# Optimization experiments

Measured on AMD Instinct MI355X. Metric: run time of the kernel, lower is better.

Reference implementation:

```python
import jax, jax.numpy as jnp
import numpy as np

VOCAB, D, H = 32000, 256, 1024
B, S = 8, 4096
PAD = 0


def setup_inputs() -> dict:
    key = jax.random.key(0)
    ks = jax.random.split(key, 9)
    x = jax.random.randint(ks[0], (B, S), 0, VOCAB)
    emb = jax.random.normal(ks[1], (VOCAB, D), jnp.float32) * 0.02
    wq = jax.random.normal(ks[2], (D, D), jnp.float32) * 0.02
    wk = jax.random.normal(ks[3], (D, D), jnp.float32) * 0.02
    wv = jax.random.normal(ks[4], (D, D), jnp.float32) * 0.02
    w1 = jax.random.normal(ks[5], (H, D), jnp.float32) * 0.02
    b1 = jnp.zeros((H,), jnp.float32)
    w2 = jax.random.normal(ks[6], (VOCAB, H), jnp.float32) * 0.02
    b2 = jnp.zeros((VOCAB,), jnp.float32)
    return {"x": x, "emb": emb, "wq": wq, "wk": wk, "wv": wv,
            "w1": w1, "b1": b1, "w2": w2, "b2": b2}


def reference(x, emb, wq, wk, wv, w1, b1, w2, b2):
    # padding_idx=0: that embedding row is zero
    emb0 = emb.at[PAD].set(0.0)
    e = emb0[x]                                   # [B,S,D]
    keep = (x != PAD).astype(e.dtype)             # 1 where key is NOT masked
    q = jnp.einsum('bsd,ed->bse', e, wq)
    k = jnp.einsum('bsd,ed->bse', e, wk)
    v = jnp.einsum('bsd,ed->bse', e, wv)
    # Original: attn = q @ k^T, masked_fill padded keys -> 0, v_out = (attn @ v).sum(dim=1)
    # Reordered (identical math, O(S*D^2) instead of O(S^2)):
    #   v_out[b,:] = (sum_i q_i) @ (sum_j keep_j * k_j v_j^T)
    qsum = q.sum(axis=1)                          # [B,D]
    kv = jnp.einsum('bsd,bse->bde', k * keep[..., None], v)  # [B,D,D]
    v_out = jnp.einsum('bd,bde->be', qsum, kv)    # [B,D]
    h = jax.nn.relu(v_out @ w1.T + b1)            # [B,H]
    logits = h @ w2.T + b2                        # [B,VOCAB]
    return jax.nn.softmax(logits, axis=-1)
```

## Files before the change

### kernel.cpp

```cpp
#include <hip/hip_runtime.h>

#define BB 8
#define SS 4096
#define DD 256
#define HH 1024
#define VOCAB 32000
#define NCH 128
#define NLB 2000

typedef float v2f __attribute__((ext_vector_type(2)));
typedef float v4f __attribute__((ext_vector_type(4)));


__global__ __launch_bounds__(256) void k_esum(const int* __restrict__ x,
        const float* __restrict__ emb, float* __restrict__ part_esum) {
    __shared__ int toks[32];
    const int b = blockIdx.y, chunk = blockIdx.x, tid = threadIdx.x;
    if (tid < 32) toks[tid] = x[b * SS + chunk * 32 + tid];
    __syncthreads();
    float acc[8];
    #pragma unroll
    for (int j = 0; j < 8; ++j) acc[j] = 0.f;
    for (int t = 0; t < 32; t += 8) {
        int tk[8];
        #pragma unroll
        for (int j = 0; j < 8; ++j) tk[j] = toks[t + j];
        #pragma unroll
        for (int j = 0; j < 8; ++j)
            if (tk[j]) acc[j] += emb[tk[j] * DD + tid];
    }
    part_esum[(b * NCH + chunk) * DD + tid] =
        ((acc[0] + acc[1]) + (acc[2] + acc[3])) + ((acc[4] + acc[5]) + (acc[6] + acc[7]));
}

__global__ __launch_bounds__(256) void k_qa(const float* __restrict__ part_esum,
        const float* __restrict__ wq, const float* __restrict__ wk,
        float* __restrict__ a) {
    const int b = blockIdx.x, tid = threadIdx.x, wid = tid >> 6, lane = tid & 63;
    __shared__ __align__(16) float red[4][DD];
    __shared__ __align__(16) float es[DD];
    __shared__ __align__(16) float qs[DD];
    {
        const v4f* p = (const v4f*)(part_esum + (size_t)b * NCH * DD) + lane;
        v4f s0 = 0.f, s1 = 0.f, s2 = 0.f, s3 = 0.f;
        #pragma unroll
        for (int k = 0; k < 32; k += 4) {
            s0 += p[(wid + 4 * (k + 0)) * 64];
            s1 += p[(wid + 4 * (k + 1)) * 64];
            s2 += p[(wid + 4 * (k + 2)) * 64];
            s3 += p[(wid + 4 * (k + 3)) * 64];
        }
        ((v4f*)red[wid])[lane] = (s0 + s1) + (s2 + s3);
    }
    __syncthreads();
    es[tid] = (red[0][tid] + red[1][tid]) + (red[2][tid] + red[3][tid]);
    __syncthreads();
    {
        const v4f es4 = ((const v4f*)es)[lane];
        for (int r0 = 0; r0 < 64; r0 += 8) {
            float dp[8];
            #pragma unroll
            for (int j = 0; j < 8; ++j) {
                const v4f w4 = ((const v4f*)(wq + (size_t)(wid * 64 + r0 + j) * DD))[lane];
                const v4f m = w4 * es4;
                dp[j] = (m.x + m.y) + (m.z + m.w);
            }
            #pragma unroll
            for (int off = 32; off; off >>= 1) {
                #pragma unroll
                for (int j = 0; j < 8; ++j) dp[j] += __shfl_xor(dp[j], off, 64);
            }
            if (lane < 8) qs[wid * 64 + r0 + lane] = dp[lane];
        }
    }
    __syncthreads();
    {
        v4f p0 = 0.f, p1 = 0.f, p2 = 0.f, p3 = 0.f;
        #pragma unroll 4
        for (int k = 0; k < 64; k += 4) {
            const int e0 = wid + 4 * k, e1 = e0 + 4, e2 = e0 + 8, e3 = e0 + 12;
            p0 += qs[e0] * ((const v4f*)(wk + (size_t)e0 * DD))[lane];
            p1 += qs[e1] * ((const v4f*)(wk + (size_t)e1 * DD))[lane];
            p2 += qs[e2] * ((const v4f*)(wk + (size_t)e2 * DD))[lane];
            p3 += qs[e3] * ((const v4f*)(wk + (size_t)e3 * DD))[lane];
        }
        ((v4f*)red[wid])[lane] = (p0 + p1) + (p2 + p3);
    }
    __syncthreads();
    a[b * DD + tid] = (red[0][tid] + red[1][tid]) + (red[2][tid] + red[3][tid]);
}

__global__ __launch_bounds__(256) void k_u(const int* __restrict__ x,
        const float* __restrict__ emb, const float* __restrict__ a,
        float* __restrict__ part_u) {
    const int b = blockIdx.y, chunk = blockIdx.x, tid = threadIdx.x;
    const int wid = tid >> 6, lane = tid & 63;
    __shared__ int toks[32];
    __shared__ __align__(16) float ured[4][DD];
    if (tid < 32) toks[tid] = x[b * SS + chunk * 32 + tid];
    __syncthreads();
    const float4 a4 = ((const float4*)(a + b * DD))[lane];
    float4 up = {0.f, 0.f, 0.f, 0.f};
    {
        int tok[8]; float4 e4[8]; float dp[8];
        #pragma unroll
        for (int j = 0; j < 8; ++j) tok[j] = toks[j * 4 + wid];
        #pragma unroll
        for (int j = 0; j < 8; ++j) {
            e4[j] = ((const float4*)(emb + tok[j] * DD))[lane];
            dp[j] = e4[j].x * a4.x + e4[j].y * a4.y + e4[j].z * a4.z + e4[j].w * a4.w;
        }
        #pragma unroll
        for (int off = 32; off; off >>= 1) {
            #pragma unroll
            for (int j = 0; j < 8; ++j) dp[j] += __shfl_xor(dp[j], off, 64);
        }
        #pragma unroll
        for (int j = 0; j < 8; ++j) {
            const float m = (tok[j] != 0) ? dp[j] : 0.f;
            up.x += m * e4[j].x; up.y += m * e4[j].y;
            up.z += m * e4[j].z; up.w += m * e4[j].w;
        }
    }
    ((float4*)ured[wid])[lane] = up;
    __syncthreads();
    part_u[(b * NCH + chunk) * DD + tid] =
        ured[0][tid] + ured[1][tid] + ured[2][tid] + ured[3][tid];
}

__global__ __launch_bounds__(256) void k_vh(const float* __restrict__ part_u,
        const float* __restrict__ wv, const float* __restrict__ w1,
        const float* __restrict__ b1, float* __restrict__ h) {
    const int b = blockIdx.y, g = blockIdx.x, tid = threadIdx.x;
    const int wid = tid >> 6, lane = tid & 63;
    __shared__ __align__(16) float red[4][DD];
    __shared__ __align__(16) float us[DD];
    __shared__ __align__(16) float vo[DD];
    {
        const v4f* p = (const v4f*)(part_u + (size_t)b * NCH * DD) + lane;
        v4f s0 = 0.f, s1 = 0.f, s2 = 0.f, s3 = 0.f;
        #pragma unroll
        for (int k = 0; k < 32; k += 4) {
            s0 += p[(wid + 4 * (k + 0)) * 64];
            s1 += p[(wid + 4 * (k + 1)) * 64];
            s2 += p[(wid + 4 * (k + 2)) * 64];
            s3 += p[(wid + 4 * (k + 3)) * 64];
        }
        ((v4f*)red[wid])[lane] = (s0 + s1) + (s2 + s3);
    }
    __syncthreads();
    us[tid] = (red[0][tid] + red[1][tid]) + (red[2][tid] + red[3][tid]);
    __syncthreads();
    {
        const v4f u4 = ((const v4f*)us)[lane];
        for (int r0 = 0; r0 < 64; r0 += 8) {
            float dp[8];
            #pragma unroll
            for (int j = 0; j < 8; ++j) {
                const v4f w4 = ((const v4f*)(wv + (size_t)(wid * 64 + r0 + j) * DD))[lane];
                const v4f m = w4 * u4;
                dp[j] = (m.x + m.y) + (m.z + m.w);
            }
            #pragma unroll
            for (int off = 32; off; off >>= 1) {
                #pragma unroll
                for (int j = 0; j < 8; ++j) dp[j] += __shfl_xor(dp[j], off, 64);
            }
            if (lane < 8) vo[wid * 64 + r0 + lane] = dp[lane];
        }
    }
    __syncthreads();
    {
        const float4 v4 = ((const float4*)vo)[lane];
        const int rbase = g * 32 + wid * 8;
        float dp[8];
        #pragma unroll
        for (int r = 0; r < 8; ++r) {
            const float4 w4 = ((const float4*)(w1 + (size_t)(rbase + r) * DD))[lane];
            dp[r] = w4.x * v4.x + w4.y * v4.y + w4.z * v4.z + w4.w * v4.w;
        }
        #pragma unroll
        for (int off = 32; off; off >>= 1) {
            #pragma unroll
            for (int r = 0; r < 8; ++r) dp[r] += __shfl_xor(dp[r], off, 64);
        }
        if (lane < 8) h[b * HH + rbase + lane] = fmaxf(dp[lane] + b1[rbase + lane], 0.f);
    }
}

__global__ __launch_bounds__(256, 4) void k_logits(const float* __restrict__ h,
        const float* __restrict__ w2, const float* __restrict__ b2,
        float* __restrict__ out, float* __restrict__ spart) {
    const int tid = threadIdx.x, wid = tid >> 6, lane = tid & 63;
    const int half = lane >> 5;
    v2f hp[16];
    #pragma unroll
    for (int c = 0; c < 4; ++c) {
        const float4 ta = ((const float4*)(h + (2 * wid)     * HH + c * 256))[lane];
        const float4 tb = ((const float4*)(h + (2 * wid + 1) * HH + c * 256))[lane];
        hp[c * 4 + 0] = (v2f){ta.x, tb.x};
        hp[c * 4 + 1] = (v2f){ta.y, tb.y};
        hp[c * 4 + 2] = (v2f){ta.z, tb.z};
        hp[c * 4 + 3] = (v2f){ta.w, tb.w};
    }
    float m_run = -1e30f, s_run = 0.f;
    #pragma unroll 2
    for (int r = 0; r < 16; ++r) {
        const int i = blockIdx.x + r * NLB;
        const float4* row = (const float4*)(w2 + (size_t)i * HH);
        v2f acc = (v2f){0.f, 0.f};
        #pragma unroll
        for (int c = 0; c < 4; ++c) {
            const float4 w = row[c * 64 + lane];
            acc += hp[c * 4 + 0] * w.x;
            acc += hp[c * 4 + 1] * w.y;
            acc += hp[c * 4 + 2] * w.z;
            acc += hp[c * 4 + 3] * w.w;
        }
        const float send = (half == 0) ? acc.y : acc.x;
        const float keep = (half == 0) ? acc.x : acc.y;
        float s = keep + __shfl_xor(send, 32, 64);
        s += __shfl_xor(s, 16, 64);
        s += __shfl_xor(s, 8, 64);
        s += __shfl_xor(s, 4, 64);
        s += __shfl_xor(s, 2, 64);
        s += __shfl_xor(s, 1, 64);
        if ((lane & 31) == 0) {
            const float lg = s + b2[i];
            out[(2 * wid + half) * VOCAB + i] = lg;
            const float mn = fmaxf(m_run, lg);
            s_run = s_run * __expf(m_run - mn) + __expf(lg - mn);
            m_run = mn;
        }
    }
    if ((lane & 31) == 0)
        ((v2f*)spart)[(2 * wid + half) * NLB + blockIdx.x] = (v2f){m_run, s_run};
}

__global__ __launch_bounds__(256) void k_norm(const float* __restrict__ spart,
        float* __restrict__ out) {
    const int b = blockIdx.y, seg = blockIdx.x, tid = threadIdx.x;
    __shared__ float rm[256], rs[256];
    const v2f* p = (const v2f*)spart + b * NLB;
    float m = -1e30f, s = 0.f;
    for (int idx = tid; idx < NLB; idx += 256) {
        const v2f t = p[idx];
        const float mn = fmaxf(m, t.x);
        s = s * __expf(m - mn) + t.y * __expf(t.x - mn);
        m = mn;
    }
    rm[tid] = m; rs[tid] = s;
    __syncthreads();
    for (int st = 128; st; st >>= 1) {
        if (tid < st) {
            const float m2 = rm[tid + st], s2 = rs[tid + st];
            const float mn = fmaxf(rm[tid], m2);
            rs[tid] = rs[tid] * __expf(rm[tid] - mn) + s2 * __expf(m2 - mn);
            rm[tid] = mn;
        }
        __syncthreads();
    }
    const float gm = rm[0], ginv = 1.f / rs[0];
    float* lg = out + b * VOCAB + seg * 2000;
    for (int i = tid; i < 2000; i += 256) lg[i] = __expf(lg[i] - gm) * ginv;
}

extern "C" void kernel_launch(void* const* d_in, const int* in_sizes, int n_in,
                              void* d_out, int out_size, void* d_ws, size_t ws_size,
                              hipStream_t stream) {
    const int*   x   = (const int*)d_in[0];
    const float* emb = (const float*)d_in[1];
    const float* wq  = (const float*)d_in[2];
    const float* wk  = (const float*)d_in[3];
    const float* wv  = (const float*)d_in[4];
    const float* w1  = (const float*)d_in[5];
    const float* b1  = (const float*)d_in[6];
    const float* w2  = (const float*)d_in[7];
    const float* b2  = (const float*)d_in[8];
    float* out = (float*)d_out;
    float* ws  = (float*)d_ws;

    float* part_esum = ws;
    float* part_u    = ws + 262144;
    float* a         = ws + 524288;
    float* h         = ws + 526336;
    float* spart     = ws + 534528;

    k_esum<<<dim3(NCH, BB), 256, 0, stream>>>(x, emb, part_esum);
    k_qa<<<BB, 256, 0, stream>>>(part_esum, wq, wk, a);
    k_u<<<dim3(NCH, BB), 256, 0, stream>>>(x, emb, a, part_u);
    k_vh<<<dim3(32, BB), 256, 0, stream>>>(part_u, wv, w1, b1, h);
    k_logits<<<NLB, 256, 0, stream>>>(h, w2, b2, out, spart);
    k_norm<<<dim3(16, BB), 256, 0, stream>>>(spart, out);
}
```

Before: 83.31 us.

## Double-buffer w2 rows into LDS via async global_load_lds in logits kernel

The logits kernel now stages w2 rows into a double-buffered shared-memory tile with direct global-to-LDS loads, prefetching the next group of four rows while the current group is computed. Block count is halved so each block handles 32 vocab rows instead of 16. This aims to hide global memory latency in the bandwidth-bound w2 streaming. The cost is 32KB of LDS per block plus a barrier per group, which lowers occupancy and parallelism.

```diff
diff --git a/kernel.cpp b/kernel.cpp
--- a/kernel.cpp
+++ b/kernel.cpp
@@ -6,10 +6,16 @@
 #define HH 1024
 #define VOCAB 32000
 #define NCH 128
-#define NLB 2000
+#define NLB 1000
 
 typedef float v2f __attribute__((ext_vector_type(2)));
 typedef float v4f __attribute__((ext_vector_type(4)));
+
+__device__ __forceinline__ void g2lds16(const float* gsrc, float* lds_dst) {
+    __builtin_amdgcn_global_load_lds(
+        (const __attribute__((address_space(1))) void*)gsrc,
+        (__attribute__((address_space(3))) void*)lds_dst, 16, 0, 0);
+}
 
 
 __global__ __launch_bounds__(256) void k_esum(const int* __restrict__ x,
@@ -193,6 +199,8 @@
         float* __restrict__ out, float* __restrict__ spart) {
     const int tid = threadIdx.x, wid = tid >> 6, lane = tid & 63;
     const int half = lane >> 5;
+    const int bx = blockIdx.x;
+    __shared__ __align__(16) float stage[2][4][HH];
     v2f hp[16];
     #pragma unroll
     for (int c = 0; c < 4; ++c) {
@@ -203,38 +211,52 @@
         hp[c * 4 + 2] = (v2f){ta.z, tb.z};
         hp[c * 4 + 3] = (v2f){ta.w, tb.w};
     }
+    #pragma unroll
+    for (int s = 0; s < 4; ++s)
+        g2lds16(w2 + (size_t)(bx + wid * NLB) * HH + s * 256 + lane * 4,
+                &stage[0][wid][s * 256]);
     float m_run = -1e30f, s_run = 0.f;
-    #pragma unroll 2
-    for (int r = 0; r < 16; ++r) {
-        const int i = blockIdx.x + r * NLB;
-        const float4* row = (const float4*)(w2 + (size_t)i * HH);
-        v2f acc = (v2f){0.f, 0.f};
-        #pragma unroll
-        for (int c = 0; c < 4; ++c) {
-            const float4 w = row[c * 64 + lane];
-            acc += hp[c * 4 + 0] * w.x;
-            acc += hp[c * 4 + 1] * w.y;
-            acc += hp[c * 4 + 2] * w.z;
-            acc += hp[c * 4 + 3] * w.w;
-        }
-        const float send = (half == 0) ? acc.y : acc.x;
-        const float keep = (half == 0) ? acc.x : acc.y;
-        float s = keep + __shfl_xor(send, 32, 64);
-        s += __shfl_xor(s, 16, 64);
-        s += __shfl_xor(s, 8, 64);
-        s += __shfl_xor(s, 4, 64);
-        s += __shfl_xor(s, 2, 64);
-        s += __shfl_xor(s, 1, 64);
-        if ((lane & 31) == 0) {
-            const float lg = s + b2[i];
-            out[(2 * wid + half) * VOCAB + i] = lg;
-            const float mn = fmaxf(m_run, lg);
-            s_run = s_run * __expf(m_run - mn) + __expf(lg - mn);
-            m_run = mn;
+    for (int g = 0; g < 8; ++g) {
+        __syncthreads();
+        if (g < 7) {
+            const int inext = bx + ((g + 1) * 4 + wid) * NLB;
+            #pragma unroll
+            for (int s = 0; s < 4; ++s)
+                g2lds16(w2 + (size_t)inext * HH + s * 256 + lane * 4,
+                        &stage[(g + 1) & 1][wid][s * 256]);
+        }
+        const float* buf = &stage[g & 1][0][0];
+        #pragma unroll 2
+        for (int j = 0; j < 4; ++j) {
+            const int i = bx + (g * 4 + j) * NLB;
+            v2f acc = (v2f){0.f, 0.f};
+            #pragma unroll
+            for (int c = 0; c < 4; ++c) {
+                const v4f w = ((const v4f*)(buf + j * HH + c * 256))[lane];
+                acc += hp[c * 4 + 0] * w.x;
+                acc += hp[c * 4 + 1] * w.y;
+                acc += hp[c * 4 + 2] * w.z;
+                acc += hp[c * 4 + 3] * w.w;
+            }
+            const float send = (half == 0) ? acc.y : acc.x;
+            const float keep = (half == 0) ? acc.x : acc.y;
+            float s = keep + __shfl_xor(send, 32, 64);
+            s += __shfl_xor(s, 16, 64);
+            s += __shfl_xor(s, 8, 64);
+            s += __shfl_xor(s, 4, 64);
+            s += __shfl_xor(s, 2, 64);
+            s += __shfl_xor(s, 1, 64);
+            if ((lane & 31) == 0) {
+                const float lg = s + b2[i];
+                out[(2 * wid + half) * VOCAB + i] = lg;
+                const float mn = fmaxf(m_run, lg);
+                s_run = s_run * __expf(m_run - mn) + __expf(lg - mn);
+                m_run = mn;
+            }
         }
     }
     if ((lane & 31) == 0)
-        ((v2f*)spart)[(2 * wid + half) * NLB + blockIdx.x] = (v2f){m_run, s_run};
+        ((v2f*)spart)[(2 * wid + half) * NLB + bx] = (v2f){m_run, s_run};
 }
 
 __global__ __launch_bounds__(256) void k_norm(const float* __restrict__ spart,
```

Result: slower. 87.25 us (+4.7%).
